# Performance work log

Measured on AMD Instinct MI355X. Metric: run time of the kernel, lower is better.

The kernel has to match this reference:

```python
import jax, jax.numpy as jnp
import numpy as np


def setup_inputs() -> dict:
    key = jax.random.key(0)
    k1, k2, k3 = jax.random.split(key, 3)
    B, S, D_IN, D_OUT, R = 4, 2048, 4096, 4096, 8
    x = jax.random.normal(k1, (B, S, D_IN), dtype=jnp.float32)
    # fixed_linear.weight: [out_features, in_features]
    weight = jax.random.normal(k2, (D_OUT, D_IN), dtype=jnp.float32) * 0.02
    # hra_u: [in_features, r] Householder vectors
    hra_u = jax.random.normal(k3, (D_IN, R), dtype=jnp.float32)
    return {"x": x, "weight": weight, "hra_u": hra_u}


def reference(x, weight, hra_u):
    # Normalize each Householder vector (column) as in the torch module.
    u = hra_u / jnp.linalg.norm(hra_u, axis=0, keepdims=True)  # [in, r]

    # Sequentially apply W <- W (I - 2 u u^T) == W - 2 (W u) u^T  (rank-1 update,
    # mathematically identical to the original's explicit [in,in] GEMM per step).
    def step(w, ui):  # w: [out, in], ui: [in]
        wu = w @ ui                      # [out]
        return w - 2.0 * jnp.outer(wu, ui), None

    new_weight, _ = jax.lax.scan(step, weight, u.T)  # scan over r reflections

    # F.linear(x, new_weight) = x @ new_weight^T, bias=False
    return jnp.einsum("bsd,od->bso", x, new_weight)
```

## Files before the change

kernel.cpp:

```cpp
#include <hip/hip_runtime.h>
#include <hip/hip_bf16.h>


#define D_IN   4096
#define D_OUT  4096
#define R_HH   8
#define M_ROWS 8192

typedef short bf16x8 __attribute__((ext_vector_type(8)));
typedef float f32x4  __attribute__((ext_vector_type(4)));

__device__ inline unsigned short f2bf(float f) {
    unsigned int x = __float_as_uint(f);
    unsigned int lsb = (x >> 16) & 1u;
    x += 0x7fffu + lsb;
    return (unsigned short)(x >> 16);
}

__device__ inline void async16(const unsigned short* g, char* l) {
    __builtin_amdgcn_global_load_lds(
        (const __attribute__((address_space(1))) void*)g,
        (__attribute__((address_space(3))) void*)l,
        16, 0, 0);
}

__global__ void colnorm_scale(const float* __restrict__ hu, float* __restrict__ Us) {
    const int j = blockIdx.x;
    float s = 0.f;
    for (int k = threadIdx.x; k < D_IN; k += 256) {
        float v = hu[k * R_HH + j];
        s += v * v;
    }
    __shared__ float red[256];
    red[threadIdx.x] = s;
    __syncthreads();
    for (int off = 128; off > 0; off >>= 1) {
        if (threadIdx.x < off) red[threadIdx.x] += red[threadIdx.x + off];
        __syncthreads();
    }
    __shared__ float sinv;
    if (threadIdx.x == 0) sinv = 1.0f / sqrtf(red[0]);
    __syncthreads();
    const float inv = sinv;
    for (int k = threadIdx.x; k < D_IN; k += 256)
        Us[k * R_HH + j] = hu[k * R_HH + j] * inv;
}

__global__ void gram(const float* __restrict__ Us, float* __restrict__ G) {
    const int i = blockIdx.x >> 3, j = blockIdx.x & 7;
    float s = 0.f;
    for (int k = threadIdx.x; k < D_IN; k += 256)
        s += Us[k * R_HH + i] * Us[k * R_HH + j];
    __shared__ float red[256];
    red[threadIdx.x] = s;
    __syncthreads();
    for (int off = 128; off > 0; off >>= 1) {
        if (threadIdx.x < off) red[threadIdx.x] += red[threadIdx.x + off];
        __syncthreads();
    }
    if (threadIdx.x == 0) G[i * R_HH + j] = red[0];
}

__global__ void wu_gemv(const float* __restrict__ W, const float* __restrict__ Us,
                        float* __restrict__ Y) {
    const int o = blockIdx.x;
    const float* wrow = W + (size_t)o * D_IN;
    float acc[8] = {0,0,0,0,0,0,0,0};
    for (int k = threadIdx.x; k < D_IN; k += 256) {
        float w = wrow[k];
        const float4* u4 = (const float4*)&Us[k * R_HH];
        float4 a = u4[0], b = u4[1];
        acc[0] += w * a.x; acc[1] += w * a.y; acc[2] += w * a.z; acc[3] += w * a.w;
        acc[4] += w * b.x; acc[5] += w * b.y; acc[6] += w * b.z; acc[7] += w * b.w;
    }
    __shared__ float red[8 * 256];
    #pragma unroll
    for (int j = 0; j < 8; j++) red[j * 256 + threadIdx.x] = acc[j];
    __syncthreads();
    for (int off = 128; off > 0; off >>= 1) {
        if (threadIdx.x < off)
            #pragma unroll
            for (int j = 0; j < 8; j++)
                red[j * 256 + threadIdx.x] += red[j * 256 + threadIdx.x + off];
        __syncthreads();
    }
    if (threadIdx.x < 8) Y[(size_t)o * R_HH + threadIdx.x] = red[threadIdx.x * 256];
}

__global__ void vcalc(const float* __restrict__ Y, const float* __restrict__ G,
                      float* __restrict__ V) {
    const int o = blockIdx.x * 256 + threadIdx.x;
    __shared__ float g[64];
    if (threadIdx.x < 64) g[threadIdx.x] = G[threadIdx.x];
    __syncthreads();
    float y[8], v[8];
    const float4* y4 = (const float4*)&Y[(size_t)o * R_HH];
    float4 a = y4[0], b = y4[1];
    y[0]=a.x; y[1]=a.y; y[2]=a.z; y[3]=a.w; y[4]=b.x; y[5]=b.y; y[6]=b.z; y[7]=b.w;
    #pragma unroll
    for (int i = 0; i < 8; i++) {
        float t = y[i];
        #pragma unroll
        for (int j = 0; j < 8; j++)
            if (j < i) t -= 2.0f * g[j * 8 + i] * v[j];
        v[i] = t;
    }
    float4* v4 = (float4*)&V[(size_t)o * R_HH];
    v4[0] = make_float4(v[0], v[1], v[2], v[3]);
    v4[1] = make_float4(v[4], v[5], v[6], v[7]);
}

__global__ void wn_cast(const float* __restrict__ W, const float* __restrict__ Us,
                        const float* __restrict__ V, unsigned short* __restrict__ Wn) {
    const int o = blockIdx.x;
    __shared__ float vs[8];
    if (threadIdx.x < 8) vs[threadIdx.x] = V[(size_t)o * R_HH + threadIdx.x];
    __syncthreads();
    float v[8];
    #pragma unroll
    for (int i = 0; i < 8; i++) v[i] = vs[i];
    const float4* wrow = (const float4*)(W + (size_t)o * D_IN);
    ushort4* wnrow = (ushort4*)(Wn + (size_t)o * D_IN);
    for (int k4 = threadIdx.x; k4 < D_IN / 4; k4 += 256) {
        float4 wv = wrow[k4];
        float wa[4] = {wv.x, wv.y, wv.z, wv.w};
        float out[4];
        #pragma unroll
        for (int e = 0; e < 4; e++) {
            const int k = k4 * 4 + e;
            const float4* u4 = (const float4*)&Us[k * R_HH];
            float4 ua = u4[0], ub = u4[1];
            float corr = v[0]*ua.x + v[1]*ua.y + v[2]*ua.z + v[3]*ua.w
                       + v[4]*ub.x + v[5]*ub.y + v[6]*ub.z + v[7]*ub.w;
            out[e] = wa[e] - 2.0f * corr;
        }
        ushort4 r;
        r.x = f2bf(out[0]); r.y = f2bf(out[1]); r.z = f2bf(out[2]); r.w = f2bf(out[3]);
        wnrow[k4] = r;
    }
}

__global__ void cast_x(const float4* __restrict__ x, ushort4* __restrict__ xb, int n4) {
    const int g = blockIdx.x * 256 + threadIdx.x;
    if (g >= n4) return;
    float4 f = x[g];
    ushort4 r;
    r.x = f2bf(f.x); r.y = f2bf(f.y); r.z = f2bf(f.z); r.w = f2bf(f.w);
    xb[g] = r;
}

__global__ __launch_bounds__(512, 2) void gemm256(
    const unsigned short* __restrict__ A,
    const unsigned short* __restrict__ B,
    float* __restrict__ C) {
    constexpr int K  = D_IN;
    constexpr int NN = D_OUT;
    constexpr int NT = K / 64;

    extern __shared__ __align__(16) char lds[];

    const int tid  = threadIdx.x;
    const int lane = tid & 63;
    const int wave = tid >> 6;

    const int bid = blockIdx.x;
    const int cpx = gridDim.x >> 3;
    const int swz = (bid & 7) * cpx + (bid >> 3);
    const int TN  = NN / 256;
    const int tm  = swz / TN, tn = swz - tm * TN;

    const size_t rA0 = (size_t)tm * 256;
    const size_t rB0 = (size_t)tn * 256;

    const int wr = (wave >> 2) * 128;
    const int wc = (wave & 3) * 64;

    const int sRow = tid >> 2;
    const int sCol = ((tid & 3) * 8) ^ ((sRow & 8) ? 16 : 0);
    const unsigned short* gA = A + (rA0 + sRow) * (size_t)K + sCol;
    const unsigned short* gB = B + (rB0 + sRow) * (size_t)K + sCol;

    auto stageA = [&](int kt, int h) {
        const unsigned short* g = gA + (size_t)(h * 128) * K + kt * 64;
        char* l = lds + (kt & 1) * 32768 + h * 8192 + tid * 16;
        async16(g, l);
        async16(g + 32, l + 16384);
    };
    auto stageB = [&](int kt, int h) {
        const unsigned short* g = gB + (size_t)(h * 128) * K + kt * 64;
        char* l = lds + 65536 + (kt & 1) * 32768 + h * 8192 + tid * 16;
        async16(g, l);
        async16(g + 32, l + 16384);
    };

    const int kb   = ((lane >> 4) * 16) ^ ((lane & 8) ? 32 : 0);
    const int rdA0 = (wr + (lane & 15)) * 64 + kb;
    const int rdB0 = 65536 + (wc + (lane & 15)) * 64 + kb;

    auto LDA = [&](int bb, int i, int s) -> bf16x8 {
        return *(const bf16x8*)(lds + bb * 32768 + s * 16384 + i * 1024 + rdA0);
    };
    auto LDB = [&](int bb, int j, int s) -> bf16x8 {
        return *(const bf16x8*)(lds + bb * 32768 + s * 16384 + j * 1024 + rdB0);
    };

    f32x4 acc[8][4];
    #pragma unroll
    for (int i = 0; i < 8; i++)
        #pragma unroll
        for (int j = 0; j < 4; j++)
            acc[i][j] = (f32x4){0.f, 0.f, 0.f, 0.f};

    stageA(0, 0); stageA(0, 1); stageB(0, 0); stageB(0, 1);
    stageB(1, 0); stageB(1, 1);
    asm volatile("s_waitcnt vmcnt(4)" ::: "memory");
    __builtin_amdgcn_s_barrier();

    bf16x8 a[4][2], b[4][2];

    #pragma unroll 2
    for (int kt = 0; kt < NT; ++kt) {
        const int bb = kt & 1;

        #pragma unroll
        for (int i = 0; i < 4; i++) { a[i][0] = LDA(bb, i, 0); a[i][1] = LDA(bb, i, 1); }
        #pragma unroll
        for (int j = 0; j < 4; j++) { b[j][0] = LDB(bb, j, 0); b[j][1] = LDB(bb, j, 1); }
        if (kt + 1 < NT) stageA(kt + 1, 0);
        __builtin_amdgcn_s_barrier();
        asm volatile("s_waitcnt lgkmcnt(0)" ::: "memory");
        __builtin_amdgcn_s_setprio(1);
        #pragma unroll
        for (int i = 0; i < 4; i++)
            #pragma unroll
            for (int j = 0; j < 2; j++) {
                acc[i][j] = __builtin_amdgcn_mfma_f32_16x16x32_bf16(a[i][0], b[j][0], acc[i][j], 0, 0, 0);
                acc[i][j] = __builtin_amdgcn_mfma_f32_16x16x32_bf16(a[i][1], b[j][1], acc[i][j], 0, 0, 0);
            }
        __builtin_amdgcn_s_setprio(0);
        __builtin_amdgcn_s_barrier();

        if (kt + 1 < NT) stageA(kt + 1, 1);
        __builtin_amdgcn_s_barrier();
        __builtin_amdgcn_s_setprio(1);
        #pragma unroll
        for (int i = 0; i < 4; i++)
            #pragma unroll
            for (int j = 2; j < 4; j++) {
                acc[i][j] = __builtin_amdgcn_mfma_f32_16x16x32_bf16(a[i][0], b[j][0], acc[i][j], 0, 0, 0);
                acc[i][j] = __builtin_amdgcn_mfma_f32_16x16x32_bf16(a[i][1], b[j][1], acc[i][j], 0, 0, 0);
            }
        __builtin_amdgcn_s_setprio(0);
        __builtin_amdgcn_s_barrier();

        #pragma unroll
        for (int i = 0; i < 4; i++) { a[i][0] = LDA(bb, 4 + i, 0); a[i][1] = LDA(bb, 4 + i, 1); }
        if (kt + 2 < NT) stageB(kt + 2, 0);
        __builtin_amdgcn_s_barrier();
        asm volatile("s_waitcnt lgkmcnt(0)" ::: "memory");
        __builtin_amdgcn_s_setprio(1);
        #pragma unroll
        for (int i = 0; i < 4; i++)
            #pragma unroll
            for (int j = 0; j < 2; j++) {
                acc[4 + i][j] = __builtin_amdgcn_mfma_f32_16x16x32_bf16(a[i][0], b[j][0], acc[4 + i][j], 0, 0, 0);
                acc[4 + i][j] = __builtin_amdgcn_mfma_f32_16x16x32_bf16(a[i][1], b[j][1], acc[4 + i][j], 0, 0, 0);
            }
        __builtin_amdgcn_s_setprio(0);
        __builtin_amdgcn_s_barrier();

        if (kt + 2 < NT) stageB(kt + 2, 1);
        __builtin_amdgcn_s_barrier();
        __builtin_amdgcn_s_setprio(1);
        #pragma unroll
        for (int i = 0; i < 4; i++)
            #pragma unroll
            for (int j = 2; j < 4; j++) {
                acc[4 + i][j] = __builtin_amdgcn_mfma_f32_16x16x32_bf16(a[i][0], b[j][0], acc[4 + i][j], 0, 0, 0);
                acc[4 + i][j] = __builtin_amdgcn_mfma_f32_16x16x32_bf16(a[i][1], b[j][1], acc[4 + i][j], 0, 0, 0);
            }
        __builtin_amdgcn_s_setprio(0);
        if (kt < NT - 2)
            asm volatile("s_waitcnt vmcnt(4)" ::: "memory");
        else
            asm volatile("s_waitcnt vmcnt(0)" ::: "memory");
        __builtin_amdgcn_s_barrier();
    }

    const int crow = (lane >> 4) * 4;
    const int ccol = lane & 15;
    #pragma unroll
    for (int i = 0; i < 8; i++) {
        #pragma unroll
        for (int j = 0; j < 4; j++) {
            size_t base = (rA0 + wr + i * 16 + crow) * (size_t)NN
                        + (rB0 + wc + j * 16 + ccol);
            #pragma unroll
            for (int r = 0; r < 4; r++)
                C[base + (size_t)r * NN] = acc[i][j][r];
        }
    }
}

extern "C" void kernel_launch(void* const* d_in, const int* in_sizes, int n_in,
                              void* d_out, int out_size, void* d_ws, size_t ws_size,
                              hipStream_t stream) {
    const float* x      = (const float*)d_in[0];
    const float* weight = (const float*)d_in[1];
    const float* hra_u  = (const float*)d_in[2];
    float* out = (float*)d_out;

    char* w = (char*)d_ws;
    unsigned short* Xb = (unsigned short*)w;
    unsigned short* Wn = (unsigned short*)(w + (size_t)64 * 1024 * 1024);
    float* Us = (float*)(w + (size_t)96 * 1024 * 1024);
    float* Y  = Us + (size_t)D_IN * R_HH;
    float* V  = Y  + (size_t)D_IN * R_HH;
    float* G  = V  + (size_t)D_IN * R_HH;

    static int attr_done = 0;
    if (!attr_done) {
        hipFuncSetAttribute((const void*)gemm256,
                            hipFuncAttributeMaxDynamicSharedMemorySize, 131072);
        attr_done = 1;
    }

    colnorm_scale<<<R_HH, 256, 0, stream>>>(hra_u, Us);
    gram<<<R_HH * R_HH, 256, 0, stream>>>(Us, G);
    wu_gemv<<<D_OUT, 256, 0, stream>>>(weight, Us, Y);
    vcalc<<<D_OUT / 256, 256, 0, stream>>>(Y, G, V);
    wn_cast<<<D_OUT, 256, 0, stream>>>(weight, Us, V, Wn);

    const int n4 = M_ROWS * D_IN / 4;
    cast_x<<<(n4 + 255) / 256, 256, 0, stream>>>((const float4*)x, (ushort4*)Xb, n4);

    gemm256<<<dim3((M_ROWS / 256) * (D_OUT / 256)), 512, 131072, stream>>>(Xb, Wn, out);
}
```

Baseline: 587.5 us.

## Fuse norm and Gram prep kernels and cut GEMM main-loop barriers

Replaces the separate column-normalize and Gram kernels with a single one-block prep kernel that computes the raw Gram matrix and inverse norms in one pass. The normalization is folded into the GEMV output and the correction vectors, so the scaled copy of the Householder vectors is never stored. In the bf16 GEMM main loop, four of the five barriers per half-iteration are dropped and the second A fragment set is loaded into separate registers before a single barrier. This reduces launch count and barrier stalls, but raises register pressure and relies on the staging order to avoid LDS overwrite races.

```diff
diff --git a/kernel.cpp b/kernel.cpp
--- a/kernel.cpp
+++ b/kernel.cpp
@@ -24,51 +24,61 @@
         16, 0, 0);
 }
 
-__global__ void colnorm_scale(const float* __restrict__ hu, float* __restrict__ Us) {
-    const int j = blockIdx.x;
-    float s = 0.f;
-    for (int k = threadIdx.x; k < D_IN; k += 256) {
-        float v = hu[k * R_HH + j];
-        s += v * v;
-    }
-    __shared__ float red[256];
-    red[threadIdx.x] = s;
-    __syncthreads();
-    for (int off = 128; off > 0; off >>= 1) {
-        if (threadIdx.x < off) red[threadIdx.x] += red[threadIdx.x + off];
-        __syncthreads();
-    }
-    __shared__ float sinv;
-    if (threadIdx.x == 0) sinv = 1.0f / sqrtf(red[0]);
-    __syncthreads();
-    const float inv = sinv;
-    for (int k = threadIdx.x; k < D_IN; k += 256)
-        Us[k * R_HH + j] = hu[k * R_HH + j] * inv;
-}
-
-__global__ void gram(const float* __restrict__ Us, float* __restrict__ G) {
-    const int i = blockIdx.x >> 3, j = blockIdx.x & 7;
-    float s = 0.f;
-    for (int k = threadIdx.x; k < D_IN; k += 256)
-        s += Us[k * R_HH + i] * Us[k * R_HH + j];
-    __shared__ float red[256];
-    red[threadIdx.x] = s;
-    __syncthreads();
-    for (int off = 128; off > 0; off >>= 1) {
-        if (threadIdx.x < off) red[threadIdx.x] += red[threadIdx.x + off];
-        __syncthreads();
-    }
-    if (threadIdx.x == 0) G[i * R_HH + j] = red[0];
-}
-
-__global__ void wu_gemv(const float* __restrict__ W, const float* __restrict__ Us,
-                        float* __restrict__ Y) {
+__global__ __launch_bounds__(1024) void prep(const float* __restrict__ hu,
+                                             float* __restrict__ G,
+                                             float* __restrict__ inv8) {
+    float d[36];
+    #pragma unroll
+    for (int p = 0; p < 36; p++) d[p] = 0.f;
+    for (int r = threadIdx.x; r < D_IN; r += 1024) {
+        const float4* h4 = (const float4*)&hu[r * R_HH];
+        float4 a = h4[0], b = h4[1];
+        float h[8] = {a.x, a.y, a.z, a.w, b.x, b.y, b.z, b.w};
+        int p = 0;
+        #pragma unroll
+        for (int i = 0; i < 8; i++)
+            #pragma unroll
+            for (int j = i; j < 8; j++)
+                d[p++] += h[i] * h[j];
+    }
+    #pragma unroll
+    for (int p = 0; p < 36; p++)
+        #pragma unroll
+        for (int off = 32; off > 0; off >>= 1)
+            d[p] += __shfl_down(d[p], off, 64);
+    __shared__ float red[16 * 36];
+    const int wave = threadIdx.x >> 6, lane = threadIdx.x & 63;
+    if (lane == 0)
+        #pragma unroll
+        for (int p = 0; p < 36; p++) red[wave * 36 + p] = d[p];
+    __syncthreads();
+    __shared__ float dd[36];
+    if (threadIdx.x < 36) {
+        float s = 0.f;
+        #pragma unroll
+        for (int w = 0; w < 16; w++) s += red[w * 36 + threadIdx.x];
+        dd[threadIdx.x] = s;
+    }
+    __syncthreads();
+    auto idx = [](int a, int b) { return a * 8 + b - (a * (a + 1)) / 2; };
+    if (threadIdx.x < 64) {
+        const int i = threadIdx.x >> 3, j = threadIdx.x & 7;
+        const int a = i < j ? i : j, b = i < j ? j : i;
+        const float gi = rsqrtf(dd[idx(i, i)]);
+        const float gj = rsqrtf(dd[idx(j, j)]);
+        G[threadIdx.x] = dd[idx(a, b)] * gi * gj;
+        if (j == 0) inv8[i] = gi;
+    }
+}
+
+__global__ void wu_gemv(const float* __restrict__ W, const float* __restrict__ hu,
+                        const float* __restrict__ inv8, float* __restrict__ Y) {
     const int o = blockIdx.x;
     const float* wrow = W + (size_t)o * D_IN;
     float acc[8] = {0,0,0,0,0,0,0,0};
     for (int k = threadIdx.x; k < D_IN; k += 256) {
         float w = wrow[k];
-        const float4* u4 = (const float4*)&Us[k * R_HH];
+        const float4* u4 = (const float4*)&hu[k * R_HH];
         float4 a = u4[0], b = u4[1];
         acc[0] += w * a.x; acc[1] += w * a.y; acc[2] += w * a.z; acc[3] += w * a.w;
         acc[4] += w * b.x; acc[5] += w * b.y; acc[6] += w * b.z; acc[7] += w * b.w;
@@ -84,7 +94,8 @@
                 red[j * 256 + threadIdx.x] += red[j * 256 + threadIdx.x + off];
         __syncthreads();
     }
-    if (threadIdx.x < 8) Y[(size_t)o * R_HH + threadIdx.x] = red[threadIdx.x * 256];
+    if (threadIdx.x < 8)
+        Y[(size_t)o * R_HH + threadIdx.x] = red[threadIdx.x * 256] * inv8[threadIdx.x];
 }
 
 __global__ void vcalc(const float* __restrict__ Y, const float* __restrict__ G,
@@ -110,11 +121,13 @@
     v4[1] = make_float4(v[4], v[5], v[6], v[7]);
 }
 
-__global__ void wn_cast(const float* __restrict__ W, const float* __restrict__ Us,
-                        const float* __restrict__ V, unsigned short* __restrict__ Wn) {
+__global__ void wn_cast(const float* __restrict__ W, const float* __restrict__ hu,
+                        const float* __restrict__ inv8, const float* __restrict__ V,
+                        unsigned short* __restrict__ Wn) {
     const int o = blockIdx.x;
     __shared__ float vs[8];
-    if (threadIdx.x < 8) vs[threadIdx.x] = V[(size_t)o * R_HH + threadIdx.x];
+    if (threadIdx.x < 8)
+        vs[threadIdx.x] = V[(size_t)o * R_HH + threadIdx.x] * inv8[threadIdx.x];
     __syncthreads();
     float v[8];
     #pragma unroll
@@ -128,7 +141,7 @@
         #pragma unroll
         for (int e = 0; e < 4; e++) {
             const int k = k4 * 4 + e;
-            const float4* u4 = (const float4*)&Us[k * R_HH];
+            const float4* u4 = (const float4*)&hu[k * R_HH];
             float4 ua = u4[0], ub = u4[1];
             float corr = v[0]*ua.x + v[1]*ua.y + v[2]*ua.z + v[3]*ua.w
                        + v[4]*ub.x + v[5]*ub.y + v[6]*ub.z + v[7]*ub.w;
@@ -216,70 +229,63 @@
     asm volatile("s_waitcnt vmcnt(4)" ::: "memory");
     __builtin_amdgcn_s_barrier();
 
-    bf16x8 a[4][2], b[4][2];
-
     #pragma unroll 2
     for (int kt = 0; kt < NT; ++kt) {
         const int bb = kt & 1;
 
-        #pragma unroll
-        for (int i = 0; i < 4; i++) { a[i][0] = LDA(bb, i, 0); a[i][1] = LDA(bb, i, 1); }
+        bf16x8 a0[4][2], a1[4][2], b[4][2];
+        #pragma unroll
+        for (int i = 0; i < 4; i++) { a0[i][0] = LDA(bb, i, 0); a0[i][1] = LDA(bb, i, 1); }
         #pragma unroll
         for (int j = 0; j < 4; j++) { b[j][0] = LDB(bb, j, 0); b[j][1] = LDB(bb, j, 1); }
         if (kt + 1 < NT) stageA(kt + 1, 0);
-        __builtin_amdgcn_s_barrier();
-        asm volatile("s_waitcnt lgkmcnt(0)" ::: "memory");
         __builtin_amdgcn_s_setprio(1);
         #pragma unroll
         for (int i = 0; i < 4; i++)
             #pragma unroll
             for (int j = 0; j < 2; j++) {
-                acc[i][j] = __builtin_amdgcn_mfma_f32_16x16x32_bf16(a[i][0], b[j][0], acc[i][j], 0, 0, 0);
-                acc[i][j] = __builtin_amdgcn_mfma_f32_16x16x32_bf16(a[i][1], b[j][1], acc[i][j], 0, 0, 0);
+                acc[i][j] = __builtin_amdgcn_mfma_f32_16x16x32_bf16(a0[i][0], b[j][0], acc[i][j], 0, 0, 0);
+                acc[i][j] = __builtin_amdgcn_mfma_f32_16x16x32_bf16(a0[i][1], b[j][1], acc[i][j], 0, 0, 0);
             }
         __builtin_amdgcn_s_setprio(0);
-        __builtin_amdgcn_s_barrier();
-
         if (kt + 1 < NT) stageA(kt + 1, 1);
-        __builtin_amdgcn_s_barrier();
         __builtin_amdgcn_s_setprio(1);
         #pragma unroll
         for (int i = 0; i < 4; i++)
             #pragma unroll
             for (int j = 2; j < 4; j++) {
-                acc[i][j] = __builtin_amdgcn_mfma_f32_16x16x32_bf16(a[i][0], b[j][0], acc[i][j], 0, 0, 0);
-                acc[i][j] = __builtin_amdgcn_mfma_f32_16x16x32_bf16(a[i][1], b[j][1], acc[i][j], 0, 0, 0);
+                acc[i][j] = __builtin_amdgcn_mfma_f32_16x16x32_bf16(a0[i][0], b[j][0], acc[i][j], 0, 0, 0);
+                acc[i][j] = __builtin_amdgcn_mfma_f32_16x16x32_bf16(a0[i][1], b[j][1], acc[i][j], 0, 0, 0);
             }
         __builtin_amdgcn_s_setprio(0);
+        #pragma unroll
+        for (int i = 0; i < 4; i++) { a1[i][0] = LDA(bb, 4 + i, 0); a1[i][1] = LDA(bb, 4 + i, 1); }
+
+        asm volatile("" ::: "memory");
         __builtin_amdgcn_s_barrier();
-
-        #pragma unroll
-        for (int i = 0; i < 4; i++) { a[i][0] = LDA(bb, 4 + i, 0); a[i][1] = LDA(bb, 4 + i, 1); }
+        asm volatile("" ::: "memory");
+
         if (kt + 2 < NT) stageB(kt + 2, 0);
-        __builtin_amdgcn_s_barrier();
-        asm volatile("s_waitcnt lgkmcnt(0)" ::: "memory");
         __builtin_amdgcn_s_setprio(1);
         #pragma unroll
         for (int i = 0; i < 4; i++)
             #pragma unroll
             for (int j = 0; j < 2; j++) {
-                acc[4 + i][j] = __builtin_amdgcn_mfma_f32_16x16x32_bf16(a[i][0], b[j][0], acc[4 + i][j], 0, 0, 0);
-                acc[4 + i][j] = __builtin_amdgcn_mfma_f32_16x16x32_bf16(a[i][1], b[j][1], acc[4 + i][j], 0, 0, 0);
+                acc[4 + i][j] = __builtin_amdgcn_mfma_f32_16x16x32_bf16(a1[i][0], b[j][0], acc[4 + i][j], 0, 0, 0);
+                acc[4 + i][j] = __builtin_amdgcn_mfma_f32_16x16x32_bf16(a1[i][1], b[j][1], acc[4 + i][j], 0, 0, 0);
             }
         __builtin_amdgcn_s_setprio(0);
-        __builtin_amdgcn_s_barrier();
-
         if (kt + 2 < NT) stageB(kt + 2, 1);
-        __builtin_amdgcn_s_barrier();
         __builtin_amdgcn_s_setprio(1);
         #pragma unroll
         for (int i = 0; i < 4; i++)
             #pragma unroll
             for (int j = 2; j < 4; j++) {
-                acc[4 + i][j] = __builtin_amdgcn_mfma_f32_16x16x32_bf16(a[i][0], b[j][0], acc[4 + i][j], 0, 0, 0);
-                acc[4 + i][j] = __builtin_amdgcn_mfma_f32_16x16x32_bf16(a[i][1], b[j][1], acc[4 + i][j], 0, 0, 0);
+                acc[4 + i][j] = __builtin_amdgcn_mfma_f32_16x16x32_bf16(a1[i][0], b[j][0], acc[4 + i][j], 0, 0, 0);
+                acc[4 + i][j] = __builtin_amdgcn_mfma_f32_16x16x32_bf16(a1[i][1], b[j][1], acc[4 + i][j], 0, 0, 0);
             }
         __builtin_amdgcn_s_setprio(0);
+
         if (kt < NT - 2)
             asm volatile("s_waitcnt vmcnt(4)" ::: "memory");
         else
@@ -313,10 +319,10 @@
     char* w = (char*)d_ws;
     unsigned short* Xb = (unsigned short*)w;
     unsigned short* Wn = (unsigned short*)(w + (size_t)64 * 1024 * 1024);
-    float* Us = (float*)(w + (size_t)96 * 1024 * 1024);
-    float* Y  = Us + (size_t)D_IN * R_HH;
-    float* V  = Y  + (size_t)D_IN * R_HH;
-    float* G  = V  + (size_t)D_IN * R_HH;
+    float* Y   = (float*)(w + (size_t)96 * 1024 * 1024);
+    float* V   = Y + (size_t)D_IN * R_HH;
+    float* G   = V + (size_t)D_IN * R_HH;
+    float* inv = G + 64;
 
     static int attr_done = 0;
     if (!attr_done) {
@@ -325,11 +331,10 @@
         attr_done = 1;
     }
 
-    colnorm_scale<<<R_HH, 256, 0, stream>>>(hra_u, Us);
-    gram<<<R_HH * R_HH, 256, 0, stream>>>(Us, G);
-    wu_gemv<<<D_OUT, 256, 0, stream>>>(weight, Us, Y);
+    prep<<<1, 1024, 0, stream>>>(hra_u, G, inv);
+    wu_gemv<<<D_OUT, 256, 0, stream>>>(weight, hra_u, inv, Y);
     vcalc<<<D_OUT / 256, 256, 0, stream>>>(Y, G, V);
-    wn_cast<<<D_OUT, 256, 0, stream>>>(weight, Us, V, Wn);
+    wn_cast<<<D_OUT, 256, 0, stream>>>(weight, hra_u, inv, V, Wn);
 
     const int n4 = M_ROWS * D_IN / 4;
     cast_x<<<(n4 + 255) / 256, 256, 0, stream>>>((const float4*)x, (ushort4*)Xb, n4);
```

Result: faster. 570.2 us (-3.0%).
